# Kernel tuning notes

Hardware: AMD Instinct MI355X
Metric: run time of the kernel (lower is better)

The kernel has to match this reference:

```python
import jax, jax.numpy as jnp
import numpy as np

D = 512      # units / model dim
H = 8        # num_heads
K = 512      # key_dim (= units in this module)
B = 8
T = 512      # decoder length
S = 512      # encoder length
EPS = 1e-3   # Keras LayerNormalization default epsilon


def _layernorm(x, g, b):
    mu = jnp.mean(x, axis=-1, keepdims=True)
    var = jnp.mean(jnp.square(x - mu), axis=-1, keepdims=True)
    return (x - mu) * jax.lax.rsqrt(var + EPS) * g + b


def _mha(q_in, kv_in, wq, bq, wk, bk, wv, bv, wo, bo, causal):
    # q_in: [B,Tq,D], kv_in: [B,Tk,D]; wq/wk/wv: [D,H,K]; wo: [H,K,D]
    q = jnp.einsum('btd,dhk->bthk', q_in, wq) + bq
    k = jnp.einsum('bsd,dhk->bshk', kv_in, wk) + bk
    v = jnp.einsum('bsd,dhk->bshk', kv_in, wv) + bv
    scores = jnp.einsum('bqhk,bshk->bhqs', q, k) / jnp.sqrt(jnp.float32(K))
    if causal:
        Tq, Tk = q.shape[1], k.shape[1]
        mask = jnp.tril(jnp.ones((Tq, Tk), dtype=bool))
        scores = jnp.where(mask[None, None], scores, jnp.finfo(scores.dtype).min)
    attn = jax.nn.softmax(scores, axis=-1)
    out = jnp.einsum('bhqs,bshk->bqhk', attn, v)
    return jnp.einsum('bqhk,hkd->bqd', out, wo) + bo


def setup_inputs() -> dict:
    key = jax.random.key(0)
    ks = jax.random.split(key, 32)
    sc = 0.02
    d = {
        'in_seq': jax.random.normal(ks[0], (B, S, D), jnp.float32),
        'out_seq': jax.random.normal(ks[1], (B, T, D), jnp.float32),
    }
    i = 2
    for pfx in ('sa', 'ca'):
        d[pfx + '_wq'] = jax.random.normal(ks[i], (D, H, K)) * sc; i += 1
        d[pfx + '_bq'] = jnp.zeros((H, K))
        d[pfx + '_wk'] = jax.random.normal(ks[i], (D, H, K)) * sc; i += 1
        d[pfx + '_bk'] = jnp.zeros((H, K))
        d[pfx + '_wv'] = jax.random.normal(ks[i], (D, H, K)) * sc; i += 1
        d[pfx + '_bv'] = jnp.zeros((H, K))
        d[pfx + '_wo'] = jax.random.normal(ks[i], (H, K, D)) * sc; i += 1
        d[pfx + '_bo'] = jnp.zeros((D,))
        d[pfx + '_lng'] = jnp.ones((D,))
        d[pfx + '_lnb'] = jnp.zeros((D,))
    d['ff_w1'] = jax.random.normal(ks[i], (D, 2 * D)) * sc; i += 1
    d['ff_b1'] = jnp.zeros((2 * D,))
    d['ff_w2'] = jax.random.normal(ks[i], (2 * D, D)) * sc; i += 1
    d['ff_b2'] = jnp.zeros((D,))
    d['ff_lng'] = jnp.ones((D,))
    d['ff_lnb'] = jnp.zeros((D,))
    return d


def reference(in_seq, out_seq,
              sa_wq, sa_bq, sa_wk, sa_bk, sa_wv, sa_bv, sa_wo, sa_bo, sa_lng, sa_lnb,
              ca_wq, ca_bq, ca_wk, ca_bk, ca_wv, ca_bv, ca_wo, ca_bo, ca_lng, ca_lnb,
              ff_w1, ff_b1, ff_w2, ff_b2, ff_lng, ff_lnb):
    # causal self-attention + add + LN
    x = out_seq
    a = _mha(x, x, sa_wq, sa_bq, sa_wk, sa_bk, sa_wv, sa_bv, sa_wo, sa_bo, causal=True)
    x = _layernorm(x + a, sa_lng, sa_lnb)
    # cross-attention + add + LN
    a = _mha(x, in_seq, ca_wq, ca_bq, ca_wk, ca_bk, ca_wv, ca_bv, ca_wo, ca_bo, causal=False)
    x = _layernorm(x + a, ca_lng, ca_lnb)
    # FFN: Dense(2D, gelu) -> Dense(D) (dropout inactive at inference) + add + LN
    h = jax.nn.gelu(x @ ff_w1 + ff_b1, approximate=False)
    x = _layernorm(x + (h @ ff_w2 + ff_b2), ff_lng, ff_lnb)
    return x
```

## Files before the change

### kernel.cpp

```cpp
#include <hip/hip_runtime.h>
#include <math.h>

#define DEV __device__ __forceinline__

typedef __bf16 bf16x8 __attribute__((ext_vector_type(8)));
typedef float f32x4 __attribute__((ext_vector_type(4)));
typedef unsigned short u16x8 __attribute__((ext_vector_type(8)));

typedef const __attribute__((address_space(1))) void gv_t;
typedef __attribute__((address_space(3))) void lv_t;

DEV unsigned short f2bf(float f){
  unsigned int u = __float_as_uint(f);
  u += 0x7fffu + ((u >> 16) & 1u);
  return (unsigned short)(u >> 16);
}
DEV float bf2f(unsigned short u){ return __uint_as_float((unsigned)u << 16); }

DEV void gload16(const void* g, void* l){
  __builtin_amdgcn_global_load_lds((gv_t*)g, (lv_t*)l, 16, 0, 0);
}

DEV void xcd_decode(int& bx, int& by, int& bz){
  const int gx = gridDim.x, gy = gridDim.y;
  const int nwg = gx * gy * gridDim.z;
  int lin = blockIdx.x + gx*(blockIdx.y + gy*blockIdx.z);
  if ((nwg & 7) == 0) lin = (lin & 7)*(nwg >> 3) + (lin >> 3);
  bx = lin % gx; const int t = lin / gx;
  by = t % gy;  bz = t / gy;
}

struct Proj3 {
  const unsigned short* A[3];
  const unsigned short* B[3];
  unsigned short*       C[3];
  const float*          bias[3];
};

__global__ __launch_bounds__(512, 2)
void qkv256(Proj3 pr)
{
  __shared__ unsigned short Ab[2][16384];
  __shared__ unsigned short Bb[2][16384];

  int bxi, byi, bzi; xcd_decode(bxi, byi, bzi);
  const int m0 = byi*256, n0 = bxi*256;
  const unsigned short* A = pr.A[bzi];
  const unsigned short* B = pr.B[bzi];
  unsigned short*       C = pr.C[bzi];
  const float*       bias = pr.bias[bzi];

  const int tid = threadIdx.x, lane = tid & 63, w = tid >> 6;
  const int wr = w >> 2, wc = w & 3;
  const int l15 = lane & 15, l4 = lane >> 4;

  const int r8  = tid >> 3;
  const int sc8 = ((tid & 7) ^ (r8 & 7)) * 8;

  auto stage = [&](int buf, int kt){
    #pragma unroll
    for (int j = 0; j < 4; j++){
      gload16(A + (size_t)(m0 + j*64 + r8)*512 + kt + sc8, &Ab[buf][j*4096 + tid*8]);
      gload16(B + (size_t)(n0 + j*64 + r8)*512 + kt + sc8, &Bb[buf][j*4096 + tid*8]);
    }
  };

  f32x4 acc[8][4] = {};

  stage(0, 0);
  __syncthreads();
  for (int t = 0; t < 8; t++){
    const int cur = t & 1;
    if (t + 1 < 8) stage(cur ^ 1, (t+1)*64);

    bf16x8 bfr[4][2];
    #pragma unroll
    for (int fc = 0; fc < 4; fc++){
      const int R = wc*64 + fc*16 + l15;
      #pragma unroll
      for (int kc = 0; kc < 2; kc++){
        const int cc = (kc*32 + l4*8) ^ ((R & 7) * 8);
        bfr[fc][kc] = *(const bf16x8*)&Bb[cur][R*64 + cc];
      }
    }
    #pragma unroll
    for (int fr = 0; fr < 8; fr++){
      bf16x8 ar[2];
      const int R = wr*128 + fr*16 + l15;
      #pragma unroll
      for (int kc = 0; kc < 2; kc++){
        const int cc = (kc*32 + l4*8) ^ ((R & 7) * 8);
        ar[kc] = *(const bf16x8*)&Ab[cur][R*64 + cc];
      }
      #pragma unroll
      for (int fc = 0; fc < 4; fc++)
        #pragma unroll
        for (int kc = 0; kc < 2; kc++)
          acc[fr][fc] = __builtin_amdgcn_mfma_f32_16x16x32_bf16(
              ar[kc], bfr[fc][kc], acc[fr][fc], 0, 0, 0);
    }
    __syncthreads();
  }

  #pragma unroll
  for (int fr = 0; fr < 8; fr++){
    const int mb = m0 + wr*128 + fr*16 + l4*4;
    #pragma unroll
    for (int fc = 0; fc < 4; fc++){
      const int n = n0 + wc*64 + fc*16 + l15;
      const float bv = bias[n];
      #pragma unroll
      for (int r = 0; r < 4; r++)
        C[(size_t)(mb + r)*4096 + n] = f2bf(acc[fr][fc][r] + bv);
    }
  }
}

template<int CMODE, int CSK>
__global__ __launch_bounds__(512, 2)
void gemm256(const unsigned short* __restrict__ A, const unsigned short* __restrict__ B,
             void* __restrict__ C, const float* __restrict__ bias,
             int M, int N, int K, int lda, int ldb, int ldc,
             size_t aOffH, size_t aOffB, size_t bOffH, size_t bOffB,
             size_t cOffH, size_t cOffB)
{
  __shared__ unsigned short Ab[2][2][8192];
  __shared__ unsigned short Bb[2][2][8192];

  int bxi, byi, bzi; xcd_decode(bxi, byi, bzi);
  const int m0 = byi*256, n0 = bxi*256;
  if (CSK == 1 && n0 > m0 + 255) return;

  const int z = bzi, bb = z >> 3, hh = z & 7;
  A += (size_t)bb*aOffB + (size_t)hh*aOffH;
  B += (size_t)bb*bOffB + (size_t)hh*bOffH;
  const size_t coff = (size_t)bb*cOffB + (size_t)hh*cOffH;

  const int tid = threadIdx.x, lane = tid & 63, w = tid >> 6;
  const int wr = w >> 2, wc = w & 3;
  const int l15 = lane & 15, l4 = lane >> 4;

  int Keff = K;
  if (CSK == 2) Keff = (m0 + 256 < K) ? (m0 + 256) : K;
  const int nt = Keff >> 6;

  const int r8  = tid >> 3;
  const int sc8 = ((tid & 7) ^ (r8 & 7)) * 8;

  auto stageA = [&](int buf, int half, int kt){
    #pragma unroll
    for (int j = 0; j < 2; j++){
      const int lr = j*64 + r8;
      gload16(A + (size_t)(m0 + half*128 + lr)*lda + kt + sc8,
              &Ab[buf][half][j*4096 + tid*8]);
    }
  };
  auto stageB = [&](int buf, int half, int kt){
    #pragma unroll
    for (int j = 0; j < 2; j++){
      const int lr = j*64 + r8;
      gload16(B + (size_t)(n0 + half*128 + lr)*ldb + kt + sc8,
              &Bb[buf][half][j*4096 + tid*8]);
    }
  };

  f32x4 acc[8][4] = {};

  stageB(0,0,0); stageB(0,1,0);
  stageA(0,0,0); stageA(0,1,0);
  if (nt > 1){
    stageA(1,0,64); stageA(1,1,64);
    stageB(1,0,64); stageB(1,1,64);
    asm volatile("s_waitcnt vmcnt(8)" ::: "memory");
  } else {
    asm volatile("s_waitcnt vmcnt(0)" ::: "memory");
  }
  __builtin_amdgcn_s_barrier();
  __builtin_amdgcn_sched_barrier(0);

  for (int Q = 0; Q < nt; Q++){
    const int cur = Q & 1;
    if (Q > 0){
      if (Q + 1 < nt) asm volatile("s_waitcnt vmcnt(4)" ::: "memory");
      else            asm volatile("s_waitcnt vmcnt(0)" ::: "memory");
      __builtin_amdgcn_s_barrier();
      __builtin_amdgcn_sched_barrier(0);
    }
    bf16x8 bfr[4][2];
    #pragma unroll
    for (int s = 0; s < 4; s++){
      if (s == 0){
        #pragma unroll
        for (int fc = 0; fc < 4; fc++){
          const int R = wc*64 + fc*16 + l15;
          const int hb = R >> 7, lr = R & 127;
          #pragma unroll
          for (int kc = 0; kc < 2; kc++){
            const int cc = (kc*32 + l4*8) ^ ((lr & 7) * 8);
            bfr[fc][kc] = *(const bf16x8*)&Bb[cur][hb][lr*64 + cc];
          }
        }
      }
      bf16x8 ar[2][2];
      #pragma unroll
      for (int f = 0; f < 2; f++){
        const int lr = (s*2 + f)*16 + l15;
        #pragma unroll
        for (int kc = 0; kc < 2; kc++){
          const int cc = (kc*32 + l4*8) ^ ((lr & 7) * 8);
          ar[f][kc] = *(const bf16x8*)&Ab[cur][wr][lr*64 + cc];
        }
      }
      if (s == 0 && Q >= 1 && Q + 1 < nt) stageA(cur ^ 1, 0, (Q+1)*64);
      if (s == 1 && Q >= 1 && Q + 1 < nt) stageA(cur ^ 1, 1, (Q+1)*64);
      if (s == 2 && Q + 2 < nt)           stageB(cur,     0, (Q+2)*64);
      if (s == 3 && Q + 2 < nt)           stageB(cur,     1, (Q+2)*64);

      asm volatile("s_waitcnt lgkmcnt(0)" ::: "memory");
      __builtin_amdgcn_sched_barrier(0);
      __builtin_amdgcn_s_setprio(1);
      #pragma unroll
      for (int f = 0; f < 2; f++)
        #pragma unroll
        for (int fc = 0; fc < 4; fc++)
          #pragma unroll
          for (int kc = 0; kc < 2; kc++)
            acc[s*2+f][fc] = __builtin_amdgcn_mfma_f32_16x16x32_bf16(
                ar[f][kc], bfr[fc][kc], acc[s*2+f][fc], 0, 0, 0);
      __builtin_amdgcn_s_setprio(0);
      __builtin_amdgcn_s_barrier();
      __builtin_amdgcn_sched_barrier(0);
    }
  }

  #pragma unroll
  for (int fr = 0; fr < 8; fr++){
    const int mb = m0 + wr*128 + fr*16 + l4*4;
    #pragma unroll
    for (int fc = 0; fc < 4; fc++){
      const int n = n0 + wc*64 + fc*16 + l15;
      const float bv = bias ? bias[n] : 0.0f;
      #pragma unroll
      for (int r = 0; r < 4; r++){
        const float v = acc[fr][fc][r] + bv;
        if (CMODE == 0) ((float*)C)[coff + (size_t)(mb + r)*ldc + n] = v;
        else            ((unsigned short*)C)[coff + (size_t)(mb + r)*ldc + n] = f2bf(v);
      }
    }
  }
}

template<int CMODE>
__global__ __launch_bounds__(256, 2)
void gemm_bt(const unsigned short* __restrict__ A, const unsigned short* __restrict__ B,
             void* __restrict__ C, const float* __restrict__ bias,
             int M, int N, int K, int lda, int ldb, int ldc)
{
  __shared__ unsigned short Ab[2][8192];
  __shared__ unsigned short Bb[2][8192];

  int bxi, byi, bzi; xcd_decode(bxi, byi, bzi);
  (void)bzi;
  const int m0 = byi*128, n0 = bxi*128;

  const int tid = threadIdx.x, lane = tid & 63, w = tid >> 6;
  const int wr = w >> 1, wc = w & 1;
  const int l15 = lane & 15, l4 = lane >> 4;
  const int nt = K >> 6;

  const int r8  = tid >> 3;
  const int sc8 = ((tid & 7) ^ (r8 & 7)) * 8;

  auto stage = [&](int buf, int kt){
    #pragma unroll
    for (int j = 0; j < 4; j++){
      gload16(A + (size_t)(m0 + j*32 + r8)*lda + kt + sc8, &Ab[buf][j*2048 + tid*8]);
      gload16(B + (size_t)(n0 + j*32 + r8)*ldb + kt + sc8, &Bb[buf][j*2048 + tid*8]);
    }
  };

  f32x4 acc[4][4] = {};

  stage(0, 0);
  __syncthreads();
  for (int t = 0; t < nt; t++){
    const int cur = t & 1;
    if (t + 1 < nt) stage(cur ^ 1, (t+1)*64);

    bf16x8 af[4][2], bfr[4][2];
    #pragma unroll
    for (int i = 0; i < 4; i++){
      const int Ra = wr*64 + i*16 + l15;
      const int Rb = wc*64 + i*16 + l15;
      #pragma unroll
      for (int kc = 0; kc < 2; kc++){
        const int ca = (kc*32 + l4*8) ^ ((Ra & 7) * 8);
        const int cb = (kc*32 + l4*8) ^ ((Rb & 7) * 8);
        af[i][kc]  = *(const bf16x8*)&Ab[cur][Ra*64 + ca];
        bfr[i][kc] = *(const bf16x8*)&Bb[cur][Rb*64 + cb];
      }
    }
    #pragma unroll
    for (int i = 0; i < 4; i++)
      #pragma unroll
      for (int jj = 0; jj < 4; jj++)
        #pragma unroll
        for (int kc = 0; kc < 2; kc++)
          acc[i][jj] = __builtin_amdgcn_mfma_f32_16x16x32_bf16(
              af[i][kc], bfr[jj][kc], acc[i][jj], 0, 0, 0);
    __syncthreads();
  }

  #pragma unroll
  for (int i = 0; i < 4; i++){
    const int mbase = m0 + wr*64 + i*16 + l4*4;
    #pragma unroll
    for (int jj = 0; jj < 4; jj++){
      const int n = n0 + wc*64 + jj*16 + l15;
      const float bv = bias ? bias[n] : 0.0f;
      #pragma unroll
      for (int r = 0; r < 4; r++){
        const int m = mbase + r;
        float v = acc[i][jj][r] + bv;
        if (CMODE == 0){
          ((float*)C)[(size_t)m*ldc + n] = v;
        } else if (CMODE == 1){
          ((unsigned short*)C)[(size_t)m*ldc + n] = f2bf(v);
        } else {
          v = 0.5f * v * (1.0f + erff(v * 0.70710678118654752f));
          ((unsigned short*)C)[(size_t)m*ldc + n] = f2bf(v);
        }
      }
    }
  }
}

template<int CAUSAL>
__global__ __launch_bounds__(256)
void softmax_rows(float* __restrict__ scores)
{
  const int row  = blockIdx.x*4 + (threadIdx.x >> 6);
  const int lane = threadIdx.x & 63;
  const int q = row & 511;
  const float* srow = scores + (size_t)row*512;
  float s[8]; float m = -1e30f;
  #pragma unroll
  for (int i = 0; i < 8; i++){
    const int col = lane*8 + i;
    float v = srow[col] * 0.044194173824159216f;
    if (CAUSAL && col > q) v = -1e30f;
    s[i] = v; m = fmaxf(m, v);
  }
  #pragma unroll
  for (int o = 32; o; o >>= 1) m = fmaxf(m, __shfl_xor(m, o));
  float p[8], sum = 0.f;
  #pragma unroll
  for (int i = 0; i < 8; i++){
    float e = __expf(s[i] - m);
    if (CAUSAL && (lane*8 + i) > q) e = 0.f;
    p[i] = e; sum += e;
  }
  #pragma unroll
  for (int o = 32; o; o >>= 1) sum += __shfl_xor(sum, o);
  const float inv = 1.0f / sum;
  unsigned short* prow = (unsigned short*)scores + (size_t)row*1024;
  #pragma unroll
  for (int i = 0; i < 8; i++) prow[lane*8 + i] = f2bf(p[i] * inv);
}

template<int WRITE_BF, int ND, int BFP>
__global__ __launch_bounds__(256)
void ln_rows(const float* __restrict__ x, const void* __restrict__ dbase,
             size_t dstride, const float* __restrict__ bias,
             const float* __restrict__ g, const float* __restrict__ bta,
             float* __restrict__ xo, unsigned short* __restrict__ xb)
{
  const int row = blockIdx.x*4 + (threadIdx.x >> 6);
  const int lane = threadIdx.x & 63;
  const float* xr = x + (size_t)row*512;
  float v[8];
  #pragma unroll
  for (int i = 0; i < 8; i++){
    const int c = lane*8 + i;
    v[i] = xr[c] + (bias ? bias[c] : 0.0f);
  }
  #pragma unroll
  for (int p = 0; p < ND; p++){
    if (BFP){
      const unsigned short* db = (const unsigned short*)dbase;
      u16x8 dv = *(const u16x8*)(db + p*dstride + (size_t)row*512 + lane*8);
      #pragma unroll
      for (int i = 0; i < 8; i++) v[i] += bf2f(dv[i]);
    } else {
      const float* db = (const float*)dbase;
      #pragma unroll
      for (int i = 0; i < 8; i++) v[i] += db[p*dstride + (size_t)row*512 + lane*8 + i];
    }
  }
  float sum = 0.f;
  #pragma unroll
  for (int i = 0; i < 8; i++) sum += v[i];
  #pragma unroll
  for (int o = 32; o; o >>= 1) sum += __shfl_xor(sum, o);
  const float mean = sum * (1.0f/512.0f);
  float s2 = 0.f;
  #pragma unroll
  for (int i = 0; i < 8; i++){ const float t = v[i] - mean; s2 += t*t; }
  #pragma unroll
  for (int o = 32; o; o >>= 1) s2 += __shfl_xor(s2, o);
  const float inv = rsqrtf(s2 * (1.0f/512.0f) + 1e-3f);
  #pragma unroll
  for (int i = 0; i < 8; i++){
    const int c = lane*8 + i;
    const float y = (v[i] - mean)*inv*g[c] + bta[c];
    xo[(size_t)row*512 + c] = y;
    if (WRITE_BF) xb[(size_t)row*512 + c] = f2bf(y);
  }
}

struct Cast2 { const float* s[2]; unsigned short* d[2]; };

__global__ __launch_bounds__(256)
void cast_bf16_k2(Cast2 a, int n)
{
  const int z = blockIdx.y;
  const int i = (blockIdx.x*256 + threadIdx.x)*4;
  if (i < n){
    const float4 v = *(const float4*)(a.s[z] + i);
    uint2 o;
    o.x = (unsigned)f2bf(v.x) | ((unsigned)f2bf(v.y) << 16);
    o.y = (unsigned)f2bf(v.z) | ((unsigned)f2bf(v.w) << 16);
    *(uint2*)(a.d[z] + i) = o;
  }
}

struct TC8 { const float* s[8]; unsigned short* d[8]; };

__global__ __launch_bounds__(256)
void transpose_cast8(TC8 a, int R, int C)
{
  __shared__ float tile[32][33];
  const int z = blockIdx.z;
  const float* src = a.s[z];
  unsigned short* dst = a.d[z];
  const int bx = blockIdx.x*32, by = blockIdx.y*32;
  const int tx = threadIdx.x & 31, ty = threadIdx.x >> 5;
  #pragma unroll
  for (int i = 0; i < 32; i += 8) tile[ty + i][tx] = src[(size_t)(by + ty + i)*C + bx + tx];
  __syncthreads();
  #pragma unroll
  for (int i = 0; i < 32; i += 8) dst[(size_t)(bx + ty + i)*R + by + tx] = f2bf(tile[tx][ty + i]);
}

__global__ __launch_bounds__(256)
void transpose_v(const unsigned short* __restrict__ src, unsigned short* __restrict__ dst)
{
  __shared__ unsigned short t[32][34];
  const int z = blockIdx.z, b = z >> 3, h = z & 7;
  const int s0 = blockIdx.y*32, k0 = blockIdx.x*32;
  const int tx = threadIdx.x & 31, ty4 = (threadIdx.x >> 5) * 4;
  #pragma unroll
  for (int i = 0; i < 4; i++)
    t[ty4 + i][tx] = src[(size_t)(b*512 + s0 + ty4 + i)*4096 + h*512 + k0 + tx];
  __syncthreads();
  unsigned short* d = dst + ((size_t)z*512 + k0)*512 + s0;
  #pragma unroll
  for (int i = 0; i < 4; i++)
    d[(size_t)(ty4 + i)*512 + tx] = t[tx][ty4 + i];
}

extern "C" void kernel_launch(void* const* d_in, const int* in_sizes, int n_in,
                              void* d_out, int out_size, void* d_ws, size_t ws_size,
                              hipStream_t stream)
{
  (void)in_sizes; (void)n_in; (void)out_size; (void)ws_size;

  const float* in_seq  = (const float*)d_in[0];
  const float* out_seq = (const float*)d_in[1];
  const float* sa_wq = (const float*)d_in[2];  const float* sa_bq = (const float*)d_in[3];
  const float* sa_wk = (const float*)d_in[4];  const float* sa_bk = (const float*)d_in[5];
  const float* sa_wv = (const float*)d_in[6];  const float* sa_bv = (const float*)d_in[7];
  const float* sa_wo = (const float*)d_in[8];  const float* sa_bo = (const float*)d_in[9];
  const float* sa_lng = (const float*)d_in[10]; const float* sa_lnb = (const float*)d_in[11];
  const float* ca_wq = (const float*)d_in[12]; const float* ca_bq = (const float*)d_in[13];
  const float* ca_wk = (const float*)d_in[14]; const float* ca_bk = (const float*)d_in[15];
  const float* ca_wv = (const float*)d_in[16]; const float* ca_bv = (const float*)d_in[17];
  const float* ca_wo = (const float*)d_in[18]; const float* ca_bo = (const float*)d_in[19];
  const float* ca_lng = (const float*)d_in[20]; const float* ca_lnb = (const float*)d_in[21];
  const float* ff_w1 = (const float*)d_in[22]; const float* ff_b1 = (const float*)d_in[23];
  const float* ff_w2 = (const float*)d_in[24]; const float* ff_b2 = (const float*)d_in[25];
  const float* ff_lng = (const float*)d_in[26]; const float* ff_lnb = (const float*)d_in[27];

  char* ws = (char*)d_ws;
  size_t off = 0;
  auto alloc = [&](size_t bytes){ char* p = ws + off; off += (bytes + 255) & ~(size_t)255; return p; };

  unsigned short* wT[8];
  for (int i = 0; i < 8; i++) wT[i] = (unsigned short*)alloc(4096ULL*512*2);
  unsigned short* w1T  = (unsigned short*)alloc(1024ULL*512*2);
  unsigned short* w2T  = (unsigned short*)alloc(512ULL*1024*2);
  unsigned short* xbf  = (unsigned short*)alloc(4096ULL*512*2);
  unsigned short* inbf = (unsigned short*)alloc(4096ULL*512*2);
  unsigned short* qb   = (unsigned short*)alloc(4096ULL*4096*2);
  unsigned short* kb   = (unsigned short*)alloc(4096ULL*4096*2);
  unsigned short* vT   = (unsigned short*)alloc(64ULL*512*512*2);
  float*          sc   = (float*)alloc(64ULL*512*512*4);
  float*          xcur = (float*)alloc(4096ULL*512*4);

  unsigned short* vb   = (unsigned short*)sc;
  unsigned short* part = (unsigned short*)sc;
  const size_t PART_STRIDE = 2097152;

  Cast2 c2{{out_seq, in_seq}, {xbf, inbf}};
  cast_bf16_k2<<<dim3(2048,2), 256, 0, stream>>>(c2, 4096*512);

  TC8 tqkv{{sa_wq, sa_wk, sa_wv, ca_wq, ca_wk, ca_wv, nullptr, nullptr},
           {wT[0], wT[1], wT[2], wT[4], wT[5], wT[6], nullptr, nullptr}};
  transpose_cast8<<<dim3(128,16,6), 256, 0, stream>>>(tqkv, 512, 4096);
  TC8 two{{sa_wo, ca_wo, nullptr,nullptr,nullptr,nullptr,nullptr,nullptr},
          {wT[3], wT[7], nullptr,nullptr,nullptr,nullptr,nullptr,nullptr}};
  transpose_cast8<<<dim3(16,128,2), 256, 0, stream>>>(two, 4096, 512);
  TC8 tw1{{ff_w1, nullptr,nullptr,nullptr,nullptr,nullptr,nullptr,nullptr},
          {w1T, nullptr,nullptr,nullptr,nullptr,nullptr,nullptr,nullptr}};
  transpose_cast8<<<dim3(32,16,1), 256, 0, stream>>>(tw1, 512, 1024);
  TC8 tw2{{ff_w2, nullptr,nullptr,nullptr,nullptr,nullptr,nullptr,nullptr},
          {w2T, nullptr,nullptr,nullptr,nullptr,nullptr,nullptr,nullptr}};
  transpose_cast8<<<dim3(16,32,1), 256, 0, stream>>>(tw2, 1024, 512);

  #define G256(MODE, CSK, Apt, Bpt, Cpt, BIAS, M, N, K, LDA, LDB, LDC, Z, aH, aB, bH, bB, cH, cB) \
    gemm256<MODE, CSK><<<dim3((N)/256,(M)/256,(Z)), 512, 0, stream>>>( \
      (const unsigned short*)(Apt), (const unsigned short*)(Bpt), (void*)(Cpt), BIAS, \
      M, N, K, LDA, LDB, LDC, aH, aB, bH, bB, cH, cB)

  Proj3 saP{{xbf, xbf, xbf}, {wT[0], wT[1], wT[2]}, {qb, kb, vb}, {sa_bq, sa_bk, sa_bv}};
  qkv256<<<dim3(16,16,3), 512, 0, stream>>>(saP);
  transpose_v<<<dim3(16,16,64), 256, 0, stream>>>(vb, vT);
  G256(0, 1, qb, kb, sc, nullptr, 512, 512, 512, 4096, 4096, 512, 64,
       512, 2097152, 512, 2097152, 262144, 2097152);
  softmax_rows<1><<<8192, 256, 0, stream>>>(sc);
  G256(1, 2, sc, vT, kb, nullptr, 512, 512, 512, 1024, 512, 4096, 64,
       524288, 4194304, 262144, 2097152, 512, 2097152);
  G256(1, 0, kb, wT[3], part, nullptr, 4096, 512, 512, 4096, 4096, 512, 8,
       512, 0, 512, 0, PART_STRIDE, 0);
  ln_rows<1, 8, 1><<<1024, 256, 0, stream>>>(out_seq, part, PART_STRIDE,
                                             sa_bo, sa_lng, sa_lnb, xcur, xbf);

  Proj3 caP{{xbf, inbf, inbf}, {wT[4], wT[5], wT[6]}, {qb, kb, vb}, {ca_bq, ca_bk, ca_bv}};
  qkv256<<<dim3(16,16,3), 512, 0, stream>>>(caP);
  transpose_v<<<dim3(16,16,64), 256, 0, stream>>>(vb, vT);
  G256(0, 0, qb, kb, sc, nullptr, 512, 512, 512, 4096, 4096, 512, 64,
       512, 2097152, 512, 2097152, 262144, 2097152);
  softmax_rows<0><<<8192, 256, 0, stream>>>(sc);
  G256(1, 0, sc, vT, kb, nullptr, 512, 512, 512, 1024, 512, 4096, 64,
       524288, 4194304, 262144, 2097152, 512, 2097152);
  G256(1, 0, kb, wT[7], part, nullptr, 4096, 512, 512, 4096, 4096, 512, 8,
       512, 0, 512, 0, PART_STRIDE, 0);
  ln_rows<1, 8, 1><<<1024, 256, 0, stream>>>(xcur, part, PART_STRIDE,
                                             ca_bo, ca_lng, ca_lnb, xcur, xbf);

  gemm_bt<2><<<dim3(8,32,1), 256, 0, stream>>>(
      xbf, w1T, (void*)qb, ff_b1, 4096, 1024, 512, 512, 512, 1024);
  G256(1, 0, qb, w2T, part, nullptr, 4096, 512, 128, 1024, 1024, 512, 8,
       128, 0, 128, 0, PART_STRIDE, 0);
  ln_rows<0, 8, 1><<<1024, 256, 0, stream>>>(xcur, part, PART_STRIDE,
                                             ff_b2, ff_lng, ff_lnb, (float*)d_out, nullptr);

  #undef G256
}
```

Before: 498.8 us.

## Split QKV GEMM staging into half-tiles with fine-grained vmcnt pipelining

Restructures the QKV projection GEMM main loop so the A and B tiles are staged in 128-row halves. Those half-tile loads are issued interleaved with four MFMA sub-phases per k-step, with B prefetched two steps ahead. Explicit vmcnt waits, raw s_barrier and setprio replace the full __syncthreads, so global-to-LDS loads overlap with matrix math. This adds scheduling complexity and more barriers per iteration, and buffer reuse must be correct because B is written into the current buffer.

```diff
diff --git a/kernel.cpp b/kernel.cpp
--- a/kernel.cpp
+++ b/kernel.cpp
@@ -40,8 +40,8 @@
 __global__ __launch_bounds__(512, 2)
 void qkv256(Proj3 pr)
 {
-  __shared__ unsigned short Ab[2][16384];
-  __shared__ unsigned short Bb[2][16384];
+  __shared__ unsigned short Ab[2][2][8192];
+  __shared__ unsigned short Bb[2][2][8192];
 
   int bxi, byi, bzi; xcd_decode(bxi, byi, bzi);
   const int m0 = byi*256, n0 = bxi*256;
@@ -57,49 +57,87 @@
   const int r8  = tid >> 3;
   const int sc8 = ((tid & 7) ^ (r8 & 7)) * 8;
 
-  auto stage = [&](int buf, int kt){
-    #pragma unroll
-    for (int j = 0; j < 4; j++){
-      gload16(A + (size_t)(m0 + j*64 + r8)*512 + kt + sc8, &Ab[buf][j*4096 + tid*8]);
-      gload16(B + (size_t)(n0 + j*64 + r8)*512 + kt + sc8, &Bb[buf][j*4096 + tid*8]);
+  auto stageA = [&](int buf, int half, int kt){
+    #pragma unroll
+    for (int j = 0; j < 2; j++){
+      const int lr = j*64 + r8;
+      gload16(A + (size_t)(m0 + half*128 + lr)*512 + kt + sc8,
+              &Ab[buf][half][j*4096 + tid*8]);
     }
   };
+  auto stageB = [&](int buf, int half, int kt){
+    #pragma unroll
+    for (int j = 0; j < 2; j++){
+      const int lr = j*64 + r8;
+      gload16(B + (size_t)(n0 + half*128 + lr)*512 + kt + sc8,
+              &Bb[buf][half][j*4096 + tid*8]);
+    }
+  };
 
   f32x4 acc[8][4] = {};
 
-  stage(0, 0);
-  __syncthreads();
-  for (int t = 0; t < 8; t++){
-    const int cur = t & 1;
-    if (t + 1 < 8) stage(cur ^ 1, (t+1)*64);
-
+  stageB(0,0,0); stageB(0,1,0);
+  stageA(0,0,0); stageA(0,1,0);
+  stageA(1,0,64); stageA(1,1,64);
+  stageB(1,0,64); stageB(1,1,64);
+  asm volatile("s_waitcnt vmcnt(8)" ::: "memory");
+  __builtin_amdgcn_s_barrier();
+  __builtin_amdgcn_sched_barrier(0);
+
+  const int nt = 8;
+  for (int Q = 0; Q < nt; Q++){
+    const int cur = Q & 1;
+    if (Q > 0){
+      if (Q + 1 < nt) asm volatile("s_waitcnt vmcnt(4)" ::: "memory");
+      else            asm volatile("s_waitcnt vmcnt(0)" ::: "memory");
+      __builtin_amdgcn_s_barrier();
+      __builtin_amdgcn_sched_barrier(0);
+    }
     bf16x8 bfr[4][2];
     #pragma unroll
-    for (int fc = 0; fc < 4; fc++){
-      const int R = wc*64 + fc*16 + l15;
-      #pragma unroll
-      for (int kc = 0; kc < 2; kc++){
-        const int cc = (kc*32 + l4*8) ^ ((R & 7) * 8);
-        bfr[fc][kc] = *(const bf16x8*)&Bb[cur][R*64 + cc];
+    for (int s = 0; s < 4; s++){
+      if (s == 0){
+        #pragma unroll
+        for (int fc = 0; fc < 4; fc++){
+          const int R = wc*64 + fc*16 + l15;
+          const int hb = R >> 7, lr = R & 127;
+          #pragma unroll
+          for (int kc = 0; kc < 2; kc++){
+            const int cc = (kc*32 + l4*8) ^ ((lr & 7) * 8);
+            bfr[fc][kc] = *(const bf16x8*)&Bb[cur][hb][lr*64 + cc];
+          }
+        }
       }
-    }
-    #pragma unroll
-    for (int fr = 0; fr < 8; fr++){
-      bf16x8 ar[2];
-      const int R = wr*128 + fr*16 + l15;
-      #pragma unroll
-      for (int kc = 0; kc < 2; kc++){
-        const int cc = (kc*32 + l4*8) ^ ((R & 7) * 8);
-        ar[kc] = *(const bf16x8*)&Ab[cur][R*64 + cc];
+      bf16x8 ar[2][2];
+      #pragma unroll
+      for (int f = 0; f < 2; f++){
+        const int lr = (s*2 + f)*16 + l15;
+        #pragma unroll
+        for (int kc = 0; kc < 2; kc++){
+          const int cc = (kc*32 + l4*8) ^ ((lr & 7) * 8);
+          ar[f][kc] = *(const bf16x8*)&Ab[cur][wr][lr*64 + cc];
+        }
       }
-      #pragma unroll
-      for (int fc = 0; fc < 4; fc++)
+      if (s == 0 && Q >= 1 && Q + 1 < nt) stageA(cur ^ 1, 0, (Q+1)*64);
+      if (s == 1 && Q >= 1 && Q + 1 < nt) stageA(cur ^ 1, 1, (Q+1)*64);
+      if (s == 2 && Q + 2 < nt)           stageB(cur,     0, (Q+2)*64);
+      if (s == 3 && Q + 2 < nt)           stageB(cur,     1, (Q+2)*64);
+
+      asm volatile("s_waitcnt lgkmcnt(0)" ::: "memory");
+      __builtin_amdgcn_sched_barrier(0);
+      __builtin_amdgcn_s_setprio(1);
+      #pragma unroll
+      for (int f = 0; f < 2; f++)
         #pragma unroll
-        for (int kc = 0; kc < 2; kc++)
-          acc[fr][fc] = __builtin_amdgcn_mfma_f32_16x16x32_bf16(
-              ar[kc], bfr[fc][kc], acc[fr][fc], 0, 0, 0);
-    }
-    __syncthreads();
+        for (int fc = 0; fc < 4; fc++)
+          #pragma unroll
+          for (int kc = 0; kc < 2; kc++)
+            acc[s*2+f][fc] = __builtin_amdgcn_mfma_f32_16x16x32_bf16(
+                ar[f][kc], bfr[fc][kc], acc[s*2+f][fc], 0, 0, 0);
+      __builtin_amdgcn_s_setprio(0);
+      __builtin_amdgcn_s_barrier();
+      __builtin_amdgcn_sched_barrier(0);
+    }
   }
 
   #pragma unroll
```

Result: no change. 490.0 us (-1.8%).
